# Performance work log

Hardware: AMD Instinct MI355X
Metric: run time of the kernel (lower is better)

Reference implementation:

```python
import jax, jax.numpy as jnp
import numpy as np

# Graph: 3-node chain 0 -> 1 -> 2, node 0 takes the external stimulus.
B, T, CIN, H, W = 8, 8, 3, 64, 64
PROJ = 32            # proj_hidden_dim
CDIM = 32            # per-node cell input_dim (integrator output channels)
HID = 64             # per-node hidden_dim
NUM_NODE = 3
PROCESS_T = T + NUM_NODE - 1  # default process_time in forward


def _conv(x, w, b):
    # 3x3, stride 1, 'same' padding, NCHW / OIHW
    y = jax.lax.conv_general_dilated(x, w, (1, 1), ((1, 1), (1, 1)),
                                     dimension_numbers=('NCHW', 'OIHW', 'NCHW'))
    return y + b[None, :, None, None]


def _gru(x, h, wg, bg, wc, bc):
    # standard ConvGRU cell (topdown branch inactive: basal/apical dims = 0)
    gates = jax.nn.sigmoid(_conv(jnp.concatenate([x, h], axis=1), wg, bg))
    r, z = jnp.split(gates, 2, axis=1)
    cand = jnp.tanh(_conv(jnp.concatenate([x, r * h], axis=1), wc, bc))
    return z * h + (1.0 - z) * cand


def setup_inputs() -> dict:
    key = jax.random.key(0)
    ks = iter(jax.random.split(key, 40))

    def w(shape):
        fan_in = shape[1] * shape[2] * shape[3]
        return jax.random.normal(next(ks), shape, jnp.float32) / np.sqrt(fan_in)

    inp = {'x': jax.random.normal(next(ks), (B, T, CIN, H, W), jnp.float32)}
    # bottomup per-edge projection convs
    inp['Win0'] = w((PROJ, CIN, 3, 3)); inp['bin0'] = jnp.zeros((PROJ,), jnp.float32)
    inp['We10'] = w((PROJ, HID, 3, 3)); inp['be10'] = jnp.zeros((PROJ,), jnp.float32)
    inp['We21'] = w((PROJ, HID, 3, 3)); inp['be21'] = jnp.zeros((PROJ,), jnp.float32)
    # per-node integrator convs + ConvGRU cell params
    for n in range(NUM_NODE):
        inp[f'Wint{n}'] = w((CDIM, PROJ, 3, 3)); inp[f'bint{n}'] = jnp.zeros((CDIM,), jnp.float32)
        inp[f'Wg{n}'] = w((2 * HID, CDIM + HID, 3, 3)); inp[f'bg{n}'] = jnp.zeros((2 * HID,), jnp.float32)
        inp[f'Wc{n}'] = w((HID, CDIM + HID, 3, 3)); inp[f'bc{n}'] = jnp.zeros((HID,), jnp.float32)
    return inp


def reference(x, Win0, bin0, We10, be10, We21, be21,
              Wint0, bint0, Wg0, bg0, Wc0, bc0,
              Wint1, bint1, Wg1, bg1, Wc1, bc1,
              Wint2, bint2, Wg2, bg2, Wc2, bc2):
    h = [jnp.zeros((B, HID, H, W), x.dtype) for _ in range(NUM_NODE)]
    h_prev = list(h)
    for t in range(PROCESS_T):
        new_h = list(h)
        # node 0: external stimulus (zeros after seq ends), becomes active at t=0
        inp = x[:, t] if t < T else jnp.zeros_like(x[:, 0])
        bu0 = _conv(_conv(inp, Win0, bin0), Wint0, bint0)
        new_h[0] = _gru(bu0, h[0], Wg0, bg0, Wc0, bc0)
        # node 1: in-edge from node 0, activates at t=1 (wave propagation)
        if t >= 1:
            bu1 = _conv(_conv(h_prev[0], We10, be10), Wint1, bint1)
            new_h[1] = _gru(bu1, h[1], Wg1, bg1, Wc1, bc1)
        # node 2: in-edge from node 1, activates at t=2
        if t >= 2:
            bu2 = _conv(_conv(h_prev[1], We21, be21), Wint2, bint2)
            new_h[2] = _gru(bu2, h[2], Wg2, bg2, Wc2, bc2)
        h = new_h
        h_prev = list(h)
    # output node index 2
    return h[2]
```

## Files before the change

### kernel.cpp

```cpp
#include <hip/hip_runtime.h>
#include <hip/hip_bf16.h>

#define BATCH 8
#define TSEQ 8
#define HH 64
#define WW 64
#define HID 64
#define PT 10
#define PIXN 32768

typedef __bf16 bf16_t;
typedef __bf16 bf16x8 __attribute__((ext_vector_type(8)));
typedef float  f32x4  __attribute__((ext_vector_type(4)));

__device__ __forceinline__ float fsigmoid(float v) {
    float e = __builtin_amdgcn_exp2f(-1.4426950408889634f * v);
    return __builtin_amdgcn_rcpf(1.0f + e);
}
__device__ __forceinline__ float ftanh(float v) {
    float e = __builtin_amdgcn_exp2f(2.8853900817779268f * v);
    return 1.0f - 2.0f * __builtin_amdgcn_rcpf(1.0f + e);
}

struct PackSeg { const float* src; bf16_t* dst; int NT16; int KC; int CinReal; int begin; };
struct PackArgs { PackSeg s[12]; int total; };

__global__ void wpack_all(PackArgs P) {
    int idx = blockIdx.x * 256 + threadIdx.x;
    if (idx >= P.total) return;
    int si = 0;
#pragma unroll
    for (int i = 1; i < 12; ++i) if (idx >= P.s[i].begin) si = i;
    PackSeg sg = P.s[si];
    int l = idx - sg.begin;
    int j    = l & 7;
    int lane = (l >> 3) & 63;
    int rest = l >> 9;
    int nt   = rest % sg.NT16;
    int chunk = rest / sg.NT16;
    int kc  = chunk % sg.KC;
    int tap = chunk / sg.KC;
    int co = nt * 16 + (lane & 15);
    int ci = kc * 32 + (lane >> 4) * 8 + j;
    float v = (ci < sg.CinReal) ? sg.src[((long)co * sg.CinReal + ci) * 9 + tap] : 0.0f;
    sg.dst[l] = (bf16_t)v;
}

struct PJ {
    const bf16_t* X;
    const float*  Xf;
    int t;
    const bf16_t* Wpj;
    const float*  bpj;
    const bf16_t* Wit;
    const float*  bit;
    bf16_t* outB;
};
struct PJs { PJ u[8]; };

template <int XIN>
__global__ __launch_bounds__(256, 2) void projint_k(PJs P) {
    constexpr int PSBX = 136;
    constexpr int PSBP = 72;
    constexpr int POFF = 6 * 66 * PSBX;
    __shared__ __align__(16) char smem[6 * 66 * PSBX + 4 * 66 * PSBP];

    const PJ u = P.u[blockIdx.y];
    const int tid = threadIdx.x, lane = tid & 63, w = tid >> 6;
    const int b = blockIdx.x & 7, y0 = (blockIdx.x >> 3) * 2;
    const int l15 = lane & 15, kg = lane >> 4;

    const bf16_t* wpp = u.Wpj + (size_t)(w & 1) * 512 + (size_t)lane * 8;
    bf16x8 ring[4];
#pragma unroll
    for (int i = 0; i < 4; ++i) ring[i] = *(const bf16x8*)(wpp + (size_t)i * 1024);

    if (XIN) {
        for (int c = tid; c < 6 * 66; c += 256) {
            int ry = c / 66, px = c - ry * 66;
            int gy = y0 + ry - 2, gx = px - 1;
            bf16x8 v0 = {};
            if ((unsigned)gy < 64u && (unsigned)gx < 64u) {
                long base = ((((long)b * TSEQ + u.t) * 3) * 64 + gy) * 64 + gx;
                v0[0] = (bf16_t)u.Xf[base];
                v0[1] = (bf16_t)u.Xf[base + 4096];
                v0[2] = (bf16_t)u.Xf[base + 8192];
            }
            char* dst = smem + (ry * 66 + px) * PSBX;
            *(bf16x8*)dst = v0;
            bf16x8 zz = {};
#pragma unroll
            for (int c2 = 1; c2 < 8; ++c2) *(bf16x8*)(dst + c2 * 16) = zz;
        }
    } else {
        for (int c = tid; c < 6 * 66 * 8; c += 256) {
            int ry = c / (66 * 8);
            int r  = c - ry * (66 * 8);
            int px = r >> 3, c2 = r & 7;
            int gy = y0 + ry - 2, gx = px - 1;
            bf16x8 v = {};
            if ((unsigned)gy < 64u && (unsigned)gx < 64u)
                v = *(const bf16x8*)(u.X + (((long)b * 64 + gy) * 64 + gx) * 64 + c2 * 8);
            *(bf16x8*)(smem + (ry * 66 + px) * PSBX + c2 * 16) = v;
        }
    }
    if (tid < 32) {
        int row = tid >> 3;
        int col = ((tid >> 2) & 1) ? 65 : 0;
        int chk = tid & 3;
        *(bf16x8*)(smem + POFF + (row * 66 + col) * PSBP + chk * 16) = (bf16x8){};
    }
    if (y0 == 0)
        for (int i = tid; i < 66 * 4; i += 256)
            *(bf16x8*)(smem + POFF + (0 * 66 + (i >> 2)) * PSBP + (i & 3) * 16) = (bf16x8){};
    if (y0 == 62)
        for (int i = tid; i < 66 * 4; i += 256)
            *(bf16x8*)(smem + POFF + (3 * 66 + (i >> 2)) * PSBP + (i & 3) * 16) = (bf16x8){};
    __syncthreads();

    const int ntp = w & 1, mtb = (w >> 1) * 8;
    f32x4 pacc[8];
    {
        float bv = u.bpj[ntp * 16 + l15];
#pragma unroll
        for (int mi = 0; mi < 8; ++mi) pacc[mi] = (f32x4){bv, bv, bv, bv};
    }
#pragma unroll
    for (int ch = 0; ch < 18; ++ch) {
        const int tap = ch >> 1, kc = ch & 1;
        const int ky = tap / 3, kx = tap % 3;
        bf16x8 bcur = ring[ch & 3];
        if (ch + 4 < 18) ring[ch & 3] = *(const bf16x8*)(wpp + (size_t)(ch + 4) * 1024);
#pragma unroll
        for (int mi = 0; mi < 8; ++mi) {
            const int mt = mtb + mi;
            const int prow = mt >> 2, xseg = mt & 3;
            const int addr = ((prow + ky) * 66 + xseg * 16 + l15 + kx) * PSBX
                           + kg * 16 + kc * 64;
            bf16x8 a = *(const bf16x8*)(smem + addr);
            pacc[mi] = __builtin_amdgcn_mfma_f32_16x16x32_bf16(a, bcur, pacc[mi], 0, 0, 0);
        }
    }
    const bf16_t* wpi = u.Wit + (size_t)(w & 1) * 512 + (size_t)lane * 8;
    bf16x8 ring2[4];
#pragma unroll
    for (int i = 0; i < 4; ++i) ring2[i] = *(const bf16x8*)(wpi + (size_t)i * 1024);
#pragma unroll
    for (int mi = 0; mi < 8; ++mi) {
        const int mt = mtb + mi;
        const int prow = mt >> 2, xseg = mt & 3;
        const int gyp = y0 - 1 + prow;
        if (gyp >= 0 && gyp < 64) {
            const int co = ntp * 16 + l15;
#pragma unroll
            for (int reg = 0; reg < 4; ++reg) {
                const int pxi = xseg * 16 + kg * 4 + reg;
                *(bf16_t*)(smem + POFF + (prow * 66 + pxi + 1) * PSBP + co * 2) =
                    (bf16_t)pacc[mi][reg];
            }
        }
    }
    __syncthreads();

    const int nti = w & 1, mtb2 = (w >> 1) * 4;
    f32x4 iacc[4];
    {
        float bv = u.bit[nti * 16 + l15];
#pragma unroll
        for (int mi = 0; mi < 4; ++mi) iacc[mi] = (f32x4){bv, bv, bv, bv};
    }
#pragma unroll
    for (int ch = 0; ch < 9; ++ch) {
        const int ky = ch / 3, kx = ch % 3;
        bf16x8 bcur = ring2[ch & 3];
        if (ch + 4 < 9) ring2[ch & 3] = *(const bf16x8*)(wpi + (size_t)(ch + 4) * 1024);
#pragma unroll
        for (int mi = 0; mi < 4; ++mi) {
            const int mt = mtb2 + mi;
            const int r2 = mt >> 2, xseg = mt & 3;
            const int addr = POFF + ((r2 + ky) * 66 + xseg * 16 + l15 + kx) * PSBP + kg * 16;
            bf16x8 a = *(const bf16x8*)(smem + addr);
            iacc[mi] = __builtin_amdgcn_mfma_f32_16x16x32_bf16(a, bcur, iacc[mi], 0, 0, 0);
        }
    }
    bf16_t* so = (bf16_t*)smem;
#pragma unroll
    for (int mi = 0; mi < 4; ++mi) {
        const int mt = mtb2 + mi;
        const int lpx0 = (mt >> 2) * 64 + (mt & 3) * 16 + kg * 4;
        const int co = nti * 16 + l15;
#pragma unroll
        for (int reg = 0; reg < 4; ++reg)
            so[(lpx0 + reg) * 40 + co] = (bf16_t)iacc[mi][reg];
    }
    __syncthreads();
    const long pixbase = ((long)b * 64 + y0) * 64;
    for (int i = tid; i < 128 * 4; i += 256) {
        const int p = i >> 2, cc = (i & 3) * 8;
        *(bf16x8*)(u.outB + (pixbase + p) * 32 + cc) = *(const bf16x8*)(so + p * 40 + cc);
    }
}

struct NP {
    const bf16_t* A0;
    const bf16_t* A1;
    const float*  Zf;
    const float*  Hf;
    const bf16_t* Hb;
    const bf16_t* Wp;
    const float*  bias;
    bf16_t* outB;
    float*  outF;
};
struct NPs { NP n[3]; };

template <int CIN0, int CIN1, int COUT, int MODE, int MINW>
__global__ __launch_bounds__(256, MINW) void mconv(NPs P)
{
    constexpr int CIN  = CIN0 + CIN1;
    constexpr int NT16 = COUT / 16;
    constexpr int NCH  = CIN / 8;
    constexpr int KC   = CIN / 32;
    constexpr int NCHUNK = 9 * KC;
    constexpr int PSB  = CIN * 2 + 8;
    constexpr int NT_W = (NT16 > 4) ? NT16 / 4 : 1;
    constexpr int NW_N = NT16 / NT_W;
    constexpr int NW_M = 4 / NW_N;
    constexpr int MT_W = 8 / NW_M;
    constexpr int PF   = 4;
    constexpr int ASMEM = 4 * 66 * PSB;
    constexpr int OSMEM = (MODE == 1 || MODE == 2) ? 128 * 68 * 4 + 128 * 72 * 2
                                                   : 128 * 69 * 4;
    constexpr int SMEM  = (ASMEM > OSMEM) ? ASMEM : OSMEM;

    const NP np   = P.n[blockIdx.y];
    const int tid  = threadIdx.x;
    const int lane = tid & 63;
    const int w    = tid >> 6;
    const int b  = blockIdx.x & 7;
    const int y0 = (blockIdx.x >> 3) * 2;

    __shared__ __align__(16) char smem[SMEM];

    const int nt0 = (w % NW_N) * NT_W;
    const int mt0 = (w / NW_N) * MT_W;
    const int l15 = lane & 15;
    const int kg  = lane >> 4;

    const bf16_t* wp0 = np.Wp + (size_t)nt0 * 512 + (size_t)lane * 8;
    bf16x8 ring[PF][NT_W];
#pragma unroll
    for (int i = 0; i < PF; ++i)
#pragma unroll
        for (int ni = 0; ni < NT_W; ++ni)
            ring[i][ni] = *(const bf16x8*)(wp0 + (size_t)i * (NT16 * 512) + ni * 512);

    for (int c = tid; c < 4 * 66 * NCH; c += 256) {
        int ry = c / (66 * NCH);
        int r  = c - ry * 66 * NCH;
        int px = r / NCH;
        int c2 = r - px * NCH;
        int gy = y0 + ry - 1, gx = px - 1;
        bf16x8 v = {};
        if ((unsigned)gy < 64u && (unsigned)gx < 64u) {
            long pix = ((long)b * 64 + gy) * 64 + gx;
            int ci = c2 * 8;
            if (CIN1 == 0 || ci < CIN0) v = *(const bf16x8*)(np.A0 + pix * CIN0 + ci);
            else                        v = *(const bf16x8*)(np.A1 + pix * CIN1 + (ci - CIN0));
        }
        *(bf16x8*)(smem + (ry * 66 + px) * PSB + c2 * 16) = v;
    }
    __syncthreads();

    int ab[3];
#pragma unroll
    for (int kx = 0; kx < 3; ++kx)
        ab[kx] = (l15 + kx) * PSB + kg * 16;

    f32x4 acc[MT_W][NT_W];
#pragma unroll
    for (int mi = 0; mi < MT_W; ++mi)
#pragma unroll
        for (int ni = 0; ni < NT_W; ++ni) {
            float bv = np.bias[(nt0 + ni) * 16 + l15];
            acc[mi][ni] = (f32x4){bv, bv, bv, bv};
        }

#pragma unroll
    for (int ch = 0; ch < NCHUNK; ++ch) {
        const int tap = ch / KC, kc = ch % KC;
        const int ky = tap / 3, kx = tap % 3;
        bf16x8 bcur[NT_W];
#pragma unroll
        for (int ni = 0; ni < NT_W; ++ni) bcur[ni] = ring[ch % PF][ni];
        if (ch + PF < NCHUNK) {
#pragma unroll
            for (int ni = 0; ni < NT_W; ++ni)
                ring[ch % PF][ni] =
                    *(const bf16x8*)(wp0 + (size_t)(ch + PF) * (NT16 * 512) + ni * 512);
        }
#pragma unroll
        for (int mi = 0; mi < MT_W; ++mi) {
            const int mt = mt0 + mi;
            const int row = mt >> 2, xseg = mt & 3;
            const int imm = (row + ky) * (66 * PSB) + xseg * (16 * PSB) + kc * 64;
            bf16x8 a = *(const bf16x8*)(smem + ab[kx] + imm);
#pragma unroll
            for (int ni = 0; ni < NT_W; ++ni)
                acc[mi][ni] = __builtin_amdgcn_mfma_f32_16x16x32_bf16(
                    a, bcur[ni], acc[mi][ni], 0, 0, 0);
        }
    }

    __syncthreads();
    const long pixbase = ((long)b * 64 + y0) * 64;

    if (MODE == 1) {
        bf16_t* srh = (bf16_t*)smem;
        float*  sz  = (float*)(smem + 128 * 72 * 2);
#pragma unroll
        for (int mi = 0; mi < MT_W; ++mi) {
            const int mt = mt0 + mi;
            const int lpx0 = (mt >> 2) * 64 + (mt & 3) * 16 + kg * 4;
#pragma unroll
            for (int ni = 0; ni < NT_W; ++ni) {
                const int co = (nt0 + ni) * 16 + l15;
#pragma unroll
                for (int reg = 0; reg < 4; ++reg) {
                    const int lpx = lpx0 + reg;
                    float s = fsigmoid(acc[mi][ni][reg]);
                    if (co < HID) {
                        float hv = (float)np.Hb[(pixbase + lpx) * HID + co];
                        srh[lpx * 72 + co] = (bf16_t)(s * hv);
                    } else {
                        sz[lpx * 68 + (co - HID)] = s;
                    }
                }
            }
        }
        __syncthreads();
        for (int i = tid; i < 128 * 8; i += 256) {
            const int p = i >> 3, cc = (i & 7) * 8;
            *(bf16x8*)(np.outB + (pixbase + p) * HID + cc) =
                *(const bf16x8*)(srh + p * 72 + cc);
        }
        for (int i = tid; i < 128 * 16; i += 256) {
            const int p = i >> 4, cc = (i & 15) * 4;
            *(f32x4*)(np.outF + (pixbase + p) * HID + cc) =
                *(const f32x4*)(sz + p * 68 + cc);
        }
    } else if (MODE == 2) {
        float*  shf = (float*)smem;
        bf16_t* shb = (bf16_t*)(smem + 128 * 68 * 4);
#pragma unroll
        for (int mi = 0; mi < MT_W; ++mi) {
            const int mt = mt0 + mi;
            const int lpx0 = (mt >> 2) * 64 + (mt & 3) * 16 + kg * 4;
#pragma unroll
            for (int ni = 0; ni < NT_W; ++ni) {
                const int co = (nt0 + ni) * 16 + l15;
#pragma unroll
                for (int reg = 0; reg < 4; ++reg) {
                    const int lpx = lpx0 + reg;
                    float cd = ftanh(acc[mi][ni][reg]);
                    float z  = np.Zf[(pixbase + lpx) * HID + co];
                    float ho = np.Hf[(pixbase + lpx) * HID + co];
                    float hn = z * ho + (1.0f - z) * cd;
                    shf[lpx * 68 + co] = hn;
                    shb[lpx * 72 + co] = (bf16_t)hn;
                }
            }
        }
        __syncthreads();
        for (int i = tid; i < 128 * 16; i += 256) {
            const int p = i >> 4, cc = (i & 15) * 4;
            *(f32x4*)(np.outF + (pixbase + p) * HID + cc) =
                *(const f32x4*)(shf + p * 68 + cc);
        }
        for (int i = tid; i < 128 * 8; i += 256) {
            const int p = i >> 3, cc = (i & 7) * 8;
            *(bf16x8*)(np.outB + (pixbase + p) * HID + cc) =
                *(const bf16x8*)(shb + p * 72 + cc);
        }
    } else {
        float* shf = (float*)smem;
#pragma unroll
        for (int mi = 0; mi < MT_W; ++mi) {
            const int mt = mt0 + mi;
            const int lpx0 = (mt >> 2) * 64 + (mt & 3) * 16 + kg * 4;
#pragma unroll
            for (int ni = 0; ni < NT_W; ++ni) {
                const int co = (nt0 + ni) * 16 + l15;
#pragma unroll
                for (int reg = 0; reg < 4; ++reg) {
                    const int lpx = lpx0 + reg;
                    float cd = ftanh(acc[mi][ni][reg]);
                    float z  = np.Zf[(pixbase + lpx) * HID + co];
                    float ho = np.Hf[(pixbase + lpx) * HID + co];
                    shf[lpx * 69 + co] = z * ho + (1.0f - z) * cd;
                }
            }
        }
        __syncthreads();
        for (int i = tid; i < 128 * 16; i += 256) {
            const int j = i >> 4;
            const int cc = (i & 15) * 4;
            const int co = j & 63, yr = j >> 6;
            f32x4 v = { shf[(yr * 64 + cc + 0) * 69 + co],
                        shf[(yr * 64 + cc + 1) * 69 + co],
                        shf[(yr * 64 + cc + 2) * 69 + co],
                        shf[(yr * 64 + cc + 3) * 69 + co] };
            *(f32x4*)(np.outF + (((long)b * 64 + co) * 64 + (y0 + yr)) * 64 + cc) = v;
        }
    }
}

extern "C" void kernel_launch(void* const* d_in, const int* in_sizes, int n_in,
                              void* d_out, int out_size, void* d_ws, size_t ws_size,
                              hipStream_t stream) {
    const float* x    = (const float*)d_in[0];
    const float* Win0 = (const float*)d_in[1];
    const float* bin0 = (const float*)d_in[2];
    const float* We10 = (const float*)d_in[3];
    const float* be10 = (const float*)d_in[4];
    const float* We21 = (const float*)d_in[5];
    const float* be21 = (const float*)d_in[6];
    const float* Wint[3] = {(const float*)d_in[7],  (const float*)d_in[13], (const float*)d_in[19]};
    const float* bint[3] = {(const float*)d_in[8],  (const float*)d_in[14], (const float*)d_in[20]};
    const float* Wg[3]   = {(const float*)d_in[9],  (const float*)d_in[15], (const float*)d_in[21]};
    const float* bg[3]   = {(const float*)d_in[10], (const float*)d_in[16], (const float*)d_in[22]};
    const float* Wc[3]   = {(const float*)d_in[11], (const float*)d_in[17], (const float*)d_in[23]};
    const float* bc[3]   = {(const float*)d_in[12], (const float*)d_in[18], (const float*)d_in[24]};
    (void)in_sizes; (void)n_in; (void)out_size; (void)ws_size;

    const long PIX  = (long)PIXN;
    const size_t HFSZ = (size_t)PIX * HID * 4;
    const size_t HBSZ = (size_t)PIX * HID * 2;
    const long PSZ  = PIX * 32;
    const long RHSZ = PIX * HID;
    const long ZSZ  = PIX * HID;

    char* wsb = (char*)d_ws;
    size_t off = 0;
    auto alloc = [&](size_t bytes) -> char* {
        char* q = wsb + off;
        off = (off + bytes + 255) & ~(size_t)255;
        return q;
    };

    float*  hF[6]; bf16_t* hB[6];
    hF[0] = (float*)alloc(HFSZ); hF[1] = (float*)alloc(HFSZ); hF[2] = (float*)alloc(HFSZ);
    hB[0] = (bf16_t*)alloc(HBSZ); hB[1] = (bf16_t*)alloc(HBSZ); hB[2] = (bf16_t*)alloc(HBSZ);
    const size_t zeroBytes = 3 * HFSZ + 3 * HBSZ;
    hF[3] = (float*)alloc(HFSZ); hF[4] = (float*)alloc(HFSZ); hF[5] = (float*)alloc(HFSZ);
    hB[3] = (bf16_t*)alloc(HBSZ); hB[4] = (bf16_t*)alloc(HBSZ); hB[5] = (bf16_t*)alloc(HBSZ);
    bf16_t* bu0 = (bf16_t*)alloc((size_t)TSEQ * PSZ * 2);
    bf16_t* bu  = (bf16_t*)alloc((size_t)3 * PSZ * 2);
    bf16_t* rh  = (bf16_t*)alloc((size_t)3 * RHSZ * 2);
    float*  zb  = (float*) alloc((size_t)3 * ZSZ * 4);
    bf16_t* WpIn0 = (bf16_t*)alloc((size_t)18432 * 2);
    bf16_t* WpE10 = (bf16_t*)alloc((size_t)18432 * 2);
    bf16_t* WpE21 = (bf16_t*)alloc((size_t)18432 * 2);
    bf16_t* WpInt[3], *WpG[3], *WpC[3];
    for (int n = 0; n < 3; ++n) WpInt[n] = (bf16_t*)alloc((size_t)9216 * 2);
    for (int n = 0; n < 3; ++n) WpG[n]   = (bf16_t*)alloc((size_t)110592 * 2);
    for (int n = 0; n < 3; ++n) WpC[n]   = (bf16_t*)alloc((size_t)55296 * 2);

    hipMemsetAsync(hF[0], 0, zeroBytes, stream);

    PackArgs PA{};
    int beg = 0;
    auto seg = [&](int i, const float* src, bf16_t* dst, int Cout, int CinPad, int CinReal) {
        PA.s[i] = {src, dst, Cout / 16, CinPad / 32, CinReal, beg};
        beg += 9 * (CinPad / 32) * (Cout / 16) * 512;
    };
    seg(0, Win0, WpIn0, 32, 64, 3);
    seg(1, We10, WpE10, 32, 64, 64);
    seg(2, We21, WpE21, 32, 64, 64);
    for (int n = 0; n < 3; ++n) seg(3 + n, Wint[n], WpInt[n], 32, 32, 32);
    for (int n = 0; n < 3; ++n) seg(6 + n, Wg[n],   WpG[n],   128, 96, 96);
    for (int n = 0; n < 3; ++n) seg(9 + n, Wc[n],   WpC[n],   64, 96, 96);
    PA.total = beg;
    wpack_all<<<(PA.total + 255) / 256, 256, 0, stream>>>(PA);

    {
        PJs PJ{};
        for (int t = 0; t < TSEQ; ++t) {
            PJ.u[t].Xf = x; PJ.u[t].t = t;
            PJ.u[t].Wpj = WpIn0; PJ.u[t].bpj = bin0;
            PJ.u[t].Wit = WpInt[0]; PJ.u[t].bit = bint[0];
            PJ.u[t].outB = bu0 + (long)t * PSZ;
        }
        projint_k<1><<<dim3(256, TSEQ), dim3(256), 0, stream>>>(PJ);
    }

    float*  hFc[3] = {hF[0], hF[1], hF[2]};
    float*  hFn[3] = {hF[3], hF[4], hF[5]};
    bf16_t* hBc[3] = {hB[0], hB[1], hB[2]};
    bf16_t* hBn[3] = {hB[3], hB[4], hB[5]};
    const bf16_t* WpE[2] = {WpE10, WpE21};
    const float*  beE[2] = {be10, be21};

    const dim3 T(256);
    const int GX = 256;

    for (int t = 0; t < PT; ++t) {
        const int nLo = (t > 7) ? (t - 7) : 0;
        const int nHi = (t < 2) ? t : 2;
        const int nAct = nHi - nLo + 1;

        if (t >= 1) {
            const int lo = (nLo > 1) ? nLo : 1;
            const int cnt = nHi - lo + 1;
            if (cnt > 0) {
                PJs PJ{};
                for (int i = 0; i < cnt; ++i) {
                    int n = lo + i;
                    PJ.u[i].X = hBc[n - 1];
                    PJ.u[i].Wpj = WpE[n - 1]; PJ.u[i].bpj = beE[n - 1];
                    PJ.u[i].Wit = WpInt[n];   PJ.u[i].bit = bint[n];
                    PJ.u[i].outB = bu + (long)n * PSZ;
                }
                projint_k<0><<<dim3(GX, cnt), T, 0, stream>>>(PJ);
            }
        }
        {
            NPs P{};
            for (int i = 0; i < nAct; ++i) {
                int n = nLo + i;
                P.n[i].A0 = (n == 0) ? (bu0 + (long)t * PSZ) : (bu + (long)n * PSZ);
                P.n[i].A1 = hBc[n]; P.n[i].Hb = hBc[n];
                P.n[i].Wp = WpG[n]; P.n[i].bias = bg[n];
                P.n[i].outB = rh + (long)n * RHSZ; P.n[i].outF = zb + (long)n * ZSZ;
            }
            mconv<32, 64, 128, 1, 3><<<dim3(GX, nAct), T, 0, stream>>>(P);
        }
        if (t < PT - 1) {
            NPs P{};
            for (int i = 0; i < nAct; ++i) {
                int n = nLo + i;
                P.n[i].A0 = (n == 0) ? (bu0 + (long)t * PSZ) : (bu + (long)n * PSZ);
                P.n[i].A1 = rh + (long)n * RHSZ;
                P.n[i].Zf = zb + (long)n * ZSZ; P.n[i].Hf = hFc[n];
                P.n[i].Wp = WpC[n]; P.n[i].bias = bc[n];
                P.n[i].outB = hBn[n]; P.n[i].outF = hFn[n];
            }
            mconv<32, 64, 64, 2, 3><<<dim3(GX, nAct), T, 0, stream>>>(P);
        } else {
            NPs P{};
            P.n[0].A0 = bu + (long)2 * PSZ;
            P.n[0].A1 = rh + (long)2 * RHSZ;
            P.n[0].Zf = zb + (long)2 * ZSZ; P.n[0].Hf = hFc[2];
            P.n[0].Wp = WpC[2]; P.n[0].bias = bc[2];
            P.n[0].outF = (float*)d_out;
            mconv<32, 64, 64, 3, 3><<<dim3(GX, 1), T, 0, stream>>>(P);
        }
        for (int n = nLo; n <= nHi; ++n) {
            if (t == PT - 1) break;
            float* tf = hFc[n]; hFc[n] = hFn[n]; hFn[n] = tf;
            bf16_t* tb = hBc[n]; hBc[n] = hBn[n]; hBn[n] = tb;
        }
    }
}
```

Before: 743.0 us.

## Shrink per-block tile to one output row and double grid size

Each block of the projection and GRU conv kernels now computes one output row instead of two, so the grid doubles from 256 to 512 blocks per node and the shared-memory halo shrinks. Warps are remapped so every warp owns all four x-segments of the single row, and the occupancy hint rises from 3 to 4 blocks per CU. The aim is more parallelism and better latency hiding on a GPU with many CUs. The cost is more halo rows reloaded per output row, and the weights are re-read by twice as many blocks.

```diff
diff --git a/kernel.cpp b/kernel.cpp
--- a/kernel.cpp
+++ b/kernel.cpp
@@ -62,12 +62,12 @@
 __global__ __launch_bounds__(256, 2) void projint_k(PJs P) {
     constexpr int PSBX = 136;
     constexpr int PSBP = 72;
-    constexpr int POFF = 6 * 66 * PSBX;
-    __shared__ __align__(16) char smem[6 * 66 * PSBX + 4 * 66 * PSBP];
+    constexpr int POFF = 5 * 66 * PSBX;
+    __shared__ __align__(16) char smem[POFF + 3 * 66 * PSBP];
 
     const PJ u = P.u[blockIdx.y];
     const int tid = threadIdx.x, lane = tid & 63, w = tid >> 6;
-    const int b = blockIdx.x & 7, y0 = (blockIdx.x >> 3) * 2;
+    const int b = blockIdx.x & 7, y0 = blockIdx.x >> 3;
     const int l15 = lane & 15, kg = lane >> 4;
 
     const bf16_t* wpp = u.Wpj + (size_t)(w & 1) * 512 + (size_t)lane * 8;
@@ -76,7 +76,7 @@
     for (int i = 0; i < 4; ++i) ring[i] = *(const bf16x8*)(wpp + (size_t)i * 1024);
 
     if (XIN) {
-        for (int c = tid; c < 6 * 66; c += 256) {
+        for (int c = tid; c < 5 * 66; c += 256) {
             int ry = c / 66, px = c - ry * 66;
             int gy = y0 + ry - 2, gx = px - 1;
             bf16x8 v0 = {};
@@ -93,7 +93,7 @@
             for (int c2 = 1; c2 < 8; ++c2) *(bf16x8*)(dst + c2 * 16) = zz;
         }
     } else {
-        for (int c = tid; c < 6 * 66 * 8; c += 256) {
+        for (int c = tid; c < 5 * 66 * 8; c += 256) {
             int ry = c / (66 * 8);
             int r  = c - ry * (66 * 8);
             int px = r >> 3, c2 = r & 7;
@@ -104,7 +104,7 @@
             *(bf16x8*)(smem + (ry * 66 + px) * PSBX + c2 * 16) = v;
         }
     }
-    if (tid < 32) {
+    if (tid < 24) {
         int row = tid >> 3;
         int col = ((tid >> 2) & 1) ? 65 : 0;
         int chk = tid & 3;
@@ -113,17 +113,17 @@
     if (y0 == 0)
         for (int i = tid; i < 66 * 4; i += 256)
             *(bf16x8*)(smem + POFF + (0 * 66 + (i >> 2)) * PSBP + (i & 3) * 16) = (bf16x8){};
-    if (y0 == 62)
+    if (y0 == 63)
         for (int i = tid; i < 66 * 4; i += 256)
-            *(bf16x8*)(smem + POFF + (3 * 66 + (i >> 2)) * PSBP + (i & 3) * 16) = (bf16x8){};
+            *(bf16x8*)(smem + POFF + (2 * 66 + (i >> 2)) * PSBP + (i & 3) * 16) = (bf16x8){};
     __syncthreads();
 
-    const int ntp = w & 1, mtb = (w >> 1) * 8;
-    f32x4 pacc[8];
+    const int ntp = w & 1, mtb = (w >> 1) * 6;
+    f32x4 pacc[6];
     {
         float bv = u.bpj[ntp * 16 + l15];
 #pragma unroll
-        for (int mi = 0; mi < 8; ++mi) pacc[mi] = (f32x4){bv, bv, bv, bv};
+        for (int mi = 0; mi < 6; ++mi) pacc[mi] = (f32x4){bv, bv, bv, bv};
     }
 #pragma unroll
     for (int ch = 0; ch < 18; ++ch) {
@@ -132,7 +132,7 @@
         bf16x8 bcur = ring[ch & 3];
         if (ch + 4 < 18) ring[ch & 3] = *(const bf16x8*)(wpp + (size_t)(ch + 4) * 1024);
 #pragma unroll
-        for (int mi = 0; mi < 8; ++mi) {
+        for (int mi = 0; mi < 6; ++mi) {
             const int mt = mtb + mi;
             const int prow = mt >> 2, xseg = mt & 3;
             const int addr = ((prow + ky) * 66 + xseg * 16 + l15 + kx) * PSBX
@@ -146,7 +146,7 @@
 #pragma unroll
     for (int i = 0; i < 4; ++i) ring2[i] = *(const bf16x8*)(wpi + (size_t)i * 1024);
 #pragma unroll
-    for (int mi = 0; mi < 8; ++mi) {
+    for (int mi = 0; mi < 6; ++mi) {
         const int mt = mtb + mi;
         const int prow = mt >> 2, xseg = mt & 3;
         const int gyp = y0 - 1 + prow;
@@ -162,12 +162,12 @@
     }
     __syncthreads();
 
-    const int nti = w & 1, mtb2 = (w >> 1) * 4;
-    f32x4 iacc[4];
+    const int nti = w & 1, mtb2 = (w >> 1) * 2;
+    f32x4 iacc[2];
     {
         float bv = u.bit[nti * 16 + l15];
 #pragma unroll
-        for (int mi = 0; mi < 4; ++mi) iacc[mi] = (f32x4){bv, bv, bv, bv};
+        for (int mi = 0; mi < 2; ++mi) iacc[mi] = (f32x4){bv, bv, bv, bv};
     }
 #pragma unroll
     for (int ch = 0; ch < 9; ++ch) {
@@ -175,19 +175,18 @@
         bf16x8 bcur = ring2[ch & 3];
         if (ch + 4 < 9) ring2[ch & 3] = *(const bf16x8*)(wpi + (size_t)(ch + 4) * 1024);
 #pragma unroll
-        for (int mi = 0; mi < 4; ++mi) {
-            const int mt = mtb2 + mi;
-            const int r2 = mt >> 2, xseg = mt & 3;
-            const int addr = POFF + ((r2 + ky) * 66 + xseg * 16 + l15 + kx) * PSBP + kg * 16;
+        for (int mi = 0; mi < 2; ++mi) {
+            const int xseg = mtb2 + mi;
+            const int addr = POFF + (ky * 66 + xseg * 16 + l15 + kx) * PSBP + kg * 16;
             bf16x8 a = *(const bf16x8*)(smem + addr);
             iacc[mi] = __builtin_amdgcn_mfma_f32_16x16x32_bf16(a, bcur, iacc[mi], 0, 0, 0);
         }
     }
     bf16_t* so = (bf16_t*)smem;
 #pragma unroll
-    for (int mi = 0; mi < 4; ++mi) {
-        const int mt = mtb2 + mi;
-        const int lpx0 = (mt >> 2) * 64 + (mt & 3) * 16 + kg * 4;
+    for (int mi = 0; mi < 2; ++mi) {
+        const int xseg = mtb2 + mi;
+        const int lpx0 = xseg * 16 + kg * 4;
         const int co = nti * 16 + l15;
 #pragma unroll
         for (int reg = 0; reg < 4; ++reg)
@@ -195,7 +194,7 @@
     }
     __syncthreads();
     const long pixbase = ((long)b * 64 + y0) * 64;
-    for (int i = tid; i < 128 * 4; i += 256) {
+    for (int i = tid; i < 64 * 4; i += 256) {
         const int p = i >> 2, cc = (i & 3) * 8;
         *(bf16x8*)(u.outB + (pixbase + p) * 32 + cc) = *(const bf16x8*)(so + p * 40 + cc);
     }
@@ -225,12 +224,11 @@
     constexpr int PSB  = CIN * 2 + 8;
     constexpr int NT_W = (NT16 > 4) ? NT16 / 4 : 1;
     constexpr int NW_N = NT16 / NT_W;
-    constexpr int NW_M = 4 / NW_N;
-    constexpr int MT_W = 8 / NW_M;
+    constexpr int MT_W = 4;
     constexpr int PF   = 4;
-    constexpr int ASMEM = 4 * 66 * PSB;
-    constexpr int OSMEM = (MODE == 1 || MODE == 2) ? 128 * 68 * 4 + 128 * 72 * 2
-                                                   : 128 * 69 * 4;
+    constexpr int ASMEM = 3 * 66 * PSB;
+    constexpr int OSMEM = (MODE == 1 || MODE == 2) ? 64 * 68 * 4 + 64 * 72 * 2
+                                                   : 64 * 69 * 4;
     constexpr int SMEM  = (ASMEM > OSMEM) ? ASMEM : OSMEM;
 
     const NP np   = P.n[blockIdx.y];
@@ -238,12 +236,11 @@
     const int lane = tid & 63;
     const int w    = tid >> 6;
     const int b  = blockIdx.x & 7;
-    const int y0 = (blockIdx.x >> 3) * 2;
+    const int y0 = blockIdx.x >> 3;
 
     __shared__ __align__(16) char smem[SMEM];
 
     const int nt0 = (w % NW_N) * NT_W;
-    const int mt0 = (w / NW_N) * MT_W;
     const int l15 = lane & 15;
     const int kg  = lane >> 4;
 
@@ -255,7 +252,7 @@
         for (int ni = 0; ni < NT_W; ++ni)
             ring[i][ni] = *(const bf16x8*)(wp0 + (size_t)i * (NT16 * 512) + ni * 512);
 
-    for (int c = tid; c < 4 * 66 * NCH; c += 256) {
+    for (int c = tid; c < 3 * 66 * NCH; c += 256) {
         int ry = c / (66 * NCH);
         int r  = c - ry * 66 * NCH;
         int px = r / NCH;
@@ -301,9 +298,7 @@
         }
 #pragma unroll
         for (int mi = 0; mi < MT_W; ++mi) {
-            const int mt = mt0 + mi;
-            const int row = mt >> 2, xseg = mt & 3;
-            const int imm = (row + ky) * (66 * PSB) + xseg * (16 * PSB) + kc * 64;
+            const int imm = ky * (66 * PSB) + mi * (16 * PSB) + kc * 64;
             bf16x8 a = *(const bf16x8*)(smem + ab[kx] + imm);
 #pragma unroll
             for (int ni = 0; ni < NT_W; ++ni)
@@ -317,11 +312,10 @@
 
     if (MODE == 1) {
         bf16_t* srh = (bf16_t*)smem;
-        float*  sz  = (float*)(smem + 128 * 72 * 2);
+        float*  sz  = (float*)(smem + 64 * 72 * 2);
 #pragma unroll
         for (int mi = 0; mi < MT_W; ++mi) {
-            const int mt = mt0 + mi;
-            const int lpx0 = (mt >> 2) * 64 + (mt & 3) * 16 + kg * 4;
+            const int lpx0 = mi * 16 + kg * 4;
 #pragma unroll
             for (int ni = 0; ni < NT_W; ++ni) {
                 const int co = (nt0 + ni) * 16 + l15;
@@ -339,23 +333,22 @@
             }
         }
         __syncthreads();
-        for (int i = tid; i < 128 * 8; i += 256) {
+        for (int i = tid; i < 64 * 8; i += 256) {
             const int p = i >> 3, cc = (i & 7) * 8;
             *(bf16x8*)(np.outB + (pixbase + p) * HID + cc) =
                 *(const bf16x8*)(srh + p * 72 + cc);
         }
-        for (int i = tid; i < 128 * 16; i += 256) {
+        for (int i = tid; i < 64 * 16; i += 256) {
             const int p = i >> 4, cc = (i & 15) * 4;
             *(f32x4*)(np.outF + (pixbase + p) * HID + cc) =
                 *(const f32x4*)(sz + p * 68 + cc);
         }
     } else if (MODE == 2) {
         float*  shf = (float*)smem;
-        bf16_t* shb = (bf16_t*)(smem + 128 * 68 * 4);
+        bf16_t* shb = (bf16_t*)(smem + 64 * 68 * 4);
 #pragma unroll
         for (int mi = 0; mi < MT_W; ++mi) {
-            const int mt = mt0 + mi;
-            const int lpx0 = (mt >> 2) * 64 + (mt & 3) * 16 + kg * 4;
+            const int lpx0 = mi * 16 + kg * 4;
 #pragma unroll
             for (int ni = 0; ni < NT_W; ++ni) {
                 const int co = (nt0 + ni) * 16 + l15;
@@ -372,12 +365,12 @@
             }
         }
         __syncthreads();
-        for (int i = tid; i < 128 * 16; i += 256) {
+        for (int i = tid; i < 64 * 16; i += 256) {
             const int p = i >> 4, cc = (i & 15) * 4;
             *(f32x4*)(np.outF + (pixbase + p) * HID + cc) =
                 *(const f32x4*)(shf + p * 68 + cc);
         }
-        for (int i = tid; i < 128 * 8; i += 256) {
+        for (int i = tid; i < 64 * 8; i += 256) {
             const int p = i >> 3, cc = (i & 7) * 8;
             *(bf16x8*)(np.outB + (pixbase + p) * HID + cc) =
                 *(const bf16x8*)(shb + p * 72 + cc);
@@ -386,8 +379,7 @@
         float* shf = (float*)smem;
 #pragma unroll
         for (int mi = 0; mi < MT_W; ++mi) {
-            const int mt = mt0 + mi;
-            const int lpx0 = (mt >> 2) * 64 + (mt & 3) * 16 + kg * 4;
+            const int lpx0 = mi * 16 + kg * 4;
 #pragma unroll
             for (int ni = 0; ni < NT_W; ++ni) {
                 const int co = (nt0 + ni) * 16 + l15;
@@ -402,15 +394,14 @@
             }
         }
         __syncthreads();
-        for (int i = tid; i < 128 * 16; i += 256) {
-            const int j = i >> 4;
+        for (int i = tid; i < 64 * 16; i += 256) {
+            const int co = i >> 4;
             const int cc = (i & 15) * 4;
-            const int co = j & 63, yr = j >> 6;
-            f32x4 v = { shf[(yr * 64 + cc + 0) * 69 + co],
-                        shf[(yr * 64 + cc + 1) * 69 + co],
-                        shf[(yr * 64 + cc + 2) * 69 + co],
-                        shf[(yr * 64 + cc + 3) * 69 + co] };
-            *(f32x4*)(np.outF + (((long)b * 64 + co) * 64 + (y0 + yr)) * 64 + cc) = v;
+            f32x4 v = { shf[(cc + 0) * 69 + co],
+                        shf[(cc + 1) * 69 + co],
+                        shf[(cc + 2) * 69 + co],
+                        shf[(cc + 3) * 69 + co] };
+            *(f32x4*)(np.outF + (((long)b * 64 + co) * 64 + y0) * 64 + cc) = v;
         }
     }
 }
@@ -483,6 +474,9 @@
     PA.total = beg;
     wpack_all<<<(PA.total + 255) / 256, 256, 0, stream>>>(PA);
 
+    const int GX = 512;
+    const dim3 T(256);
+
     {
         PJs PJ{};
         for (int t = 0; t < TSEQ; ++t) {
@@ -491,7 +485,7 @@
             PJ.u[t].Wit = WpInt[0]; PJ.u[t].bit = bint[0];
             PJ.u[t].outB = bu0 + (long)t * PSZ;
         }
-        projint_k<1><<<dim3(256, TSEQ), dim3(256), 0, stream>>>(PJ);
+        projint_k<1><<<dim3(GX, TSEQ), T, 0, stream>>>(PJ);
     }
 
     float*  hFc[3] = {hF[0], hF[1], hF[2]};
@@ -500,9 +494,6 @@
     bf16_t* hBn[3] = {hB[3], hB[4], hB[5]};
     const bf16_t* WpE[2] = {WpE10, WpE21};
     const float*  beE[2] = {be10, be21};
-
-    const dim3 T(256);
-    const int GX = 256;
 
     for (int t = 0; t < PT; ++t) {
         const int nLo = (t > 7) ? (t - 7) : 0;
@@ -533,7 +524,7 @@
                 P.n[i].Wp = WpG[n]; P.n[i].bias = bg[n];
                 P.n[i].outB = rh + (long)n * RHSZ; P.n[i].outF = zb + (long)n * ZSZ;
             }
-            mconv<32, 64, 128, 1, 3><<<dim3(GX, nAct), T, 0, stream>>>(P);
+            mconv<32, 64, 128, 1, 4><<<dim3(GX, nAct), T, 0, stream>>>(P);
         }
         if (t < PT - 1) {
             NPs P{};
@@ -545,7 +536,7 @@
                 P.n[i].Wp = WpC[n]; P.n[i].bias = bc[n];
                 P.n[i].outB = hBn[n]; P.n[i].outF = hFn[n];
             }
-            mconv<32, 64, 64, 2, 3><<<dim3(GX, nAct), T, 0, stream>>>(P);
+            mconv<32, 64, 64, 2, 4><<<dim3(GX, nAct), T, 0, stream>>>(P);
         } else {
             NPs P{};
             P.n[0].A0 = bu + (long)2 * PSZ;
@@ -553,7 +544,7 @@
             P.n[0].Zf = zb + (long)2 * ZSZ; P.n[0].Hf = hFc[2];
             P.n[0].Wp = WpC[2]; P.n[0].bias = bc[2];
             P.n[0].outF = (float*)d_out;
-            mconv<32, 64, 64, 3, 3><<<dim3(GX, 1), T, 0, stream>>>(P);
+            mconv<32, 64, 64, 3, 4><<<dim3(GX, 1), T, 0, stream>>>(P);
         }
         for (int n = nLo; n <= nHi; ++n) {
             if (t == PT - 1) break;
```

Result: slower. 763.7 us (+2.8%).
